# Kernel tuning notes

Measured on AMD Instinct MI355X. Metric: run time of the kernel, lower is better.

## Reference

```python
import jax, jax.numpy as jnp
import numpy as np

HEADS = 16
KEY_SIZE = 64
HEAD_SIZE = 64
D_MODEL = 1024
MASK_BIG = 1e12


def setup_inputs() -> dict:
    key = jax.random.key(0)
    ks = jax.random.split(key, 16)
    B, S, D = 4, 2048, D_MODEL
    qk_dim = HEADS * KEY_SIZE
    out_dim = HEADS * HEAD_SIZE
    s = 0.02
    return {
        'q': jax.random.normal(ks[0], (B, S, D), jnp.float32),
        'k': jax.random.normal(ks[1], (B, S, D), jnp.float32),
        'v': jax.random.normal(ks[2], (B, S, D), jnp.float32),
        'q_mask': jax.random.randint(ks[3], (B, S), 0, 2, jnp.int32),
        'v_mask': jax.random.randint(ks[4], (B, S), 0, 2, jnp.int32),
        'Wq': jax.random.normal(ks[5], (D, qk_dim), jnp.float32) * s,
        'bq': jnp.zeros((qk_dim,), jnp.float32),
        'Wk': jax.random.normal(ks[6], (D, qk_dim), jnp.float32) * s,
        'bk': jnp.zeros((qk_dim,), jnp.float32),
        'Wv': jax.random.normal(ks[7], (D, out_dim), jnp.float32) * s,
        'bv': jnp.zeros((out_dim,), jnp.float32),
        'Wo': jax.random.normal(ks[8], (out_dim, out_dim), jnp.float32) * s,
        'bo': jnp.zeros((out_dim,), jnp.float32),
    }


def reference(q, k, v, q_mask, v_mask, Wq, bq, Wk, bk, Wv, bv, Wo, bo):
    B, Sq, _ = q.shape
    Sk = k.shape[1]
    # projections -> [B, H, S, d]
    qw = (q @ Wq + bq).reshape(B, Sq, HEADS, KEY_SIZE).transpose(0, 2, 1, 3)
    kw = (k @ Wk + bk).reshape(B, Sk, HEADS, KEY_SIZE).transpose(0, 2, 1, 3)
    vw = (v @ Wv + bv).reshape(B, Sk, HEADS, HEAD_SIZE).transpose(0, 2, 1, 3)
    # scaled dot-product scores [B, H, Sq, Sk]
    a = jnp.einsum('bhqd,bhkd->bhqk', qw, kw) / np.sqrt(KEY_SIZE).astype(np.float32)
    # v_mask: additive -inf-like penalty on padded keys (mode=1, axis=-1)
    vm = v_mask.astype(a.dtype)[:, None, None, :]
    a = a - (1.0 - vm) * MASK_BIG
    # a_mask=True: causal mask (mask future positions)
    causal = jnp.tril(jnp.ones((Sq, Sk), a.dtype))
    a = a - (1.0 - causal) * MASK_BIG
    a = jax.nn.softmax(a, axis=-1)
    # attention output [B, Sq, H*head_size]
    o = jnp.einsum('bhqk,bhkd->bhqd', a, vw).transpose(0, 2, 1, 3).reshape(B, Sq, HEADS * HEAD_SIZE)
    o = o @ Wo + bo
    # q_mask: multiplicative zeroing of padded query outputs (mode=0, axis=1)
    o = o * q_mask.astype(o.dtype)[:, :, None]
    return o
```

## Files before the change

kernel.cpp:

```cpp
#include <hip/hip_runtime.h>
#include <hip/hip_bf16.h>

typedef __attribute__((ext_vector_type(8))) short v8s;
typedef __attribute__((ext_vector_type(4))) float v4f;
typedef __attribute__((ext_vector_type(16))) float v16f;
typedef __attribute__((ext_vector_type(4))) unsigned v4u;

#define S_LEN 2048
#define NB 4
#define NH 16
#define LOG2E 1.4426950408889634f
#define CMASK 1443109011456.0f
#define DEFER_THR 11.55f

__device__ __forceinline__ short f2bf(float f) {
    __hip_bfloat16 h = __float2bfloat16(f);
    union { __hip_bfloat16 h; short s; } u; u.h = h; return u.s;
}

__device__ __forceinline__ unsigned cvtpk(float lo, float hi) {
    unsigned r;
    asm("v_cvt_pk_bf16_f32 %0, %1, %2" : "=v"(r) : "v"(lo), "v"(hi));
    return r;
}

__device__ __forceinline__ int swz(int row, int col) {
    return (row * 128 + col) ^ ((row & 7) << 4);
}

__device__ __forceinline__ void async16(void* lds, const void* g) {
    __builtin_amdgcn_global_load_lds(
        (const __attribute__((address_space(1))) unsigned int*)g,
        (__attribute__((address_space(3))) unsigned int*)lds, 16, 0, 0);
}

#define MFMA16(a, b, c) __builtin_amdgcn_mfma_f32_16x16x32_bf16((a), (b), (c), 0, 0, 0)
#define MFMA32(a, b, c) __builtin_amdgcn_mfma_f32_32x32x16_bf16((a), (b), (c), 0, 0, 0)

__global__ __launch_bounds__(256) void convert_all(const float* __restrict__ q,
                                                   const float* __restrict__ k,
                                                   const float* __restrict__ v,
                                                   short* __restrict__ Xq,
                                                   short* __restrict__ Xk,
                                                   short* __restrict__ Xv,
                                                   float* __restrict__ outz) {
    if (blockIdx.y == 3) {
        size_t i = ((size_t)blockIdx.x * 256 + threadIdx.x) * 8;
        float4 z4 = {0.f, 0.f, 0.f, 0.f};
        *(float4*)(outz + i) = z4;
        *(float4*)(outz + i + 4) = z4;
        return;
    }
    const float* in = (blockIdx.y == 0) ? q : (blockIdx.y == 1) ? k : v;
    short* out = (blockIdx.y == 0) ? Xq : (blockIdx.y == 1) ? Xk : Xv;
    size_t i = ((size_t)blockIdx.x * 256 + threadIdx.x) * 8;
    float4 a = *(const float4*)(in + i);
    float4 b = *(const float4*)(in + i + 4);
    v8s o;
    o[0] = f2bf(a.x); o[1] = f2bf(a.y); o[2] = f2bf(a.z); o[3] = f2bf(a.w);
    o[4] = f2bf(b.x); o[5] = f2bf(b.y); o[6] = f2bf(b.z); o[7] = f2bf(b.w);
    *(v8s*)(out + i) = o;
}

__global__ __launch_bounds__(256) void build_pen(const int* __restrict__ vm,
                                                 short* __restrict__ penC) {
    int i = blockIdx.x * 256 + threadIdx.x;
    penC[i] = vm[i] ? (short)0 : f2bf(-CMASK);
}

__global__ __launch_bounds__(256) void compact_qmask(const int* __restrict__ qm,
                                                     int* __restrict__ idx,
                                                     int* __restrict__ nq) {
    const int b = blockIdx.x;
    const int* m = qm + b * S_LEN;
    int* ib = idx + b * S_LEN;
    __shared__ int cnt[256];
    const int t = threadIdx.x;
    int loc[8], c = 0;
#pragma unroll
    for (int i = 0; i < 8; ++i) { int s = t * 8 + i; if (m[s]) loc[c++] = s; }
    cnt[t] = c;
    __syncthreads();
    for (int d = 1; d < 256; d <<= 1) {
        int v = (t >= d) ? cnt[t - d] : 0;
        __syncthreads();
        cnt[t] += v;
        __syncthreads();
    }
    int off = cnt[t] - c;
    for (int i = 0; i < c; ++i) ib[off + i] = loc[i];
    if (t == 255) nq[b] = cnt[255];
}

__global__ __launch_bounds__(256) void transpose_all(const float* __restrict__ Wq,
                                                     const float* __restrict__ Wk,
                                                     const float* __restrict__ Wv,
                                                     const float* __restrict__ Wo,
                                                     short* __restrict__ WTq,
                                                     short* __restrict__ WTk,
                                                     short* __restrict__ WTv,
                                                     short* __restrict__ WTo) {
    const int z = blockIdx.z;
    const float* W = (z == 0) ? Wq : (z == 1) ? Wk : (z == 2) ? Wv : Wo;
    short* WT = (z == 0) ? WTq : (z == 1) ? WTk : (z == 2) ? WTv : WTo;
    __shared__ float tile[32][33];
    int k0 = blockIdx.x * 32, n0 = blockIdx.y * 32;
    int tx = threadIdx.x & 31, ty = threadIdx.x >> 5;
#pragma unroll
    for (int i = 0; i < 4; ++i)
        tile[ty + i * 8][tx] = W[(size_t)(k0 + ty + i * 8) * 1024 + n0 + tx];
    __syncthreads();
#pragma unroll
    for (int i = 0; i < 4; ++i)
        WT[(size_t)(n0 + ty + i * 8) * 1024 + k0 + tx] = f2bf(tile[tx][ty + i * 8]);
}

__global__ __launch_bounds__(512)
void proj_all(const short* __restrict__ Xk, const short* __restrict__ Xv,
              const short* __restrict__ Xq,
              const short* __restrict__ WTk, const short* __restrict__ WTv,
              const short* __restrict__ WTq,
              const float* __restrict__ bk, const float* __restrict__ bv,
              const float* __restrict__ bq,
              const int* __restrict__ idx, const int* __restrict__ nq,
              short* __restrict__ KF, short* __restrict__ VF,
              short* __restrict__ QW) {
    __shared__ short As[2][128 * 64];
    __shared__ short Bs[2][128 * 64];
    const int tid = threadIdx.x;
    const int l = tid & 63, w = tid >> 6;
    const int g = l >> 4, ql = l & 15;
    const int z = blockIdx.z;
    const int bid = blockIdx.x;
    const int y = (bid & 7) + 8 * (bid >> 6);
    const int n0 = ((bid >> 3) & 7) * 128;
    const int wr = w >> 2, wc = w & 3;

    int b = 0, m0 = y * 128, m0c = 0, nqv = 0;
    const int* idxb = nullptr;
    if (z == 2) {
        if (y >= 36) return;
        b = y / 9; m0c = (y % 9) * 128;
        nqv = nq[b];
        if (m0c >= nqv) return;
        idxb = idx + b * S_LEN;
    }
    const short* A  = (z == 0) ? Xk : (z == 1) ? Xv : Xq;
    const short* BT = (z == 0) ? WTk : (z == 1) ? WTv : WTq;
    const float* bias = (z == 0) ? bk : (z == 1) ? bv : bq;

    int arow[2];
#pragma unroll
    for (int i = 0; i < 2; ++i) {
        int row = (i * 512 + tid) >> 3;
        if (z == 2) {
            int jc = m0c + row;
            arow[i] = b * S_LEN + idxb[(jc < nqv) ? jc : (nqv - 1)];
        } else {
            arow[i] = m0 + row;
        }
    }
    const int c8 = (((l & 7) ^ (l >> 3))) * 8;

    v4f acc[4][2] = {};

    auto stage = [&](int kt, int buf) {
        const int kk = kt * 64;
#pragma unroll
        for (int i = 0; i < 2; ++i) {
            int ci = i * 512 + tid;
            async16((char*)As[buf] + (size_t)ci * 16,
                    A + (size_t)arow[i] * 1024 + kk + c8);
            async16((char*)Bs[buf] + (size_t)ci * 16,
                    BT + (size_t)(n0 + (ci >> 3)) * 1024 + kk + c8);
        }
    };

    stage(0, 0);
    for (int kt = 0; kt < 16; ++kt) {
        __builtin_amdgcn_s_barrier();
        __builtin_amdgcn_sched_barrier(0);
        if (kt + 1 < 16) {
            stage(kt + 1, (kt + 1) & 1);
            asm volatile("s_waitcnt vmcnt(4)" ::: "memory");
        } else {
            asm volatile("s_waitcnt vmcnt(0)" ::: "memory");
        }
        __builtin_amdgcn_sched_barrier(0);
        __builtin_amdgcn_s_barrier();
        __builtin_amdgcn_sched_barrier(0);
        const short* Ab = As[kt & 1];
        const short* Bb = Bs[kt & 1];
#pragma unroll
        for (int ks = 0; ks < 2; ++ks) {
            v8s af[4], bfr[2];
#pragma unroll
            for (int mt = 0; mt < 4; ++mt)
                af[mt] = *(const v8s*)((char*)Ab +
                          swz(wr * 64 + mt * 16 + ql, ks * 64 + g * 16));
#pragma unroll
            for (int nt = 0; nt < 2; ++nt)
                bfr[nt] = *(const v8s*)((char*)Bb +
                          swz(wc * 32 + nt * 16 + ql, ks * 64 + g * 16));
#pragma unroll
            for (int mt = 0; mt < 4; ++mt)
#pragma unroll
                for (int nt = 0; nt < 2; ++nt)
                    acc[mt][nt] = MFMA16(af[mt], bfr[nt], acc[mt][nt]);
        }
    }

#pragma unroll
    for (int nt = 0; nt < 2; ++nt) {
        int col = n0 + wc * 32 + nt * 16 + ql;
        float bval = bias[col];
        int hh = col >> 6, dd = col & 63;
#pragma unroll
        for (int mt = 0; mt < 4; ++mt) {
#pragma unroll
            for (int r = 0; r < 4; ++r) {
                int lrow = wr * 64 + mt * 16 + g * 4 + r;
                float vv = acc[mt][nt][r] + bval;
                if (z == 0) {
                    int gm = m0 + lrow;
                    int bb = gm >> 11, ss = gm & 2047;
                    size_t base = (size_t)(bb * NH + hh) * 131072
                                + (size_t)(ss >> 6) * 4096
                                + (dd >> 4) * 1024 + (ss & 63) * 16
                                + ((dd >> 3) & 1) * 8 + (dd & 7);
                    KF[base] = f2bf(vv);
                } else if (z == 1) {
                    int gm = m0 + lrow;
                    int bb = gm >> 11, ss = gm & 2047;
                    int wkp = ss & 63;
                    size_t base = (size_t)(bb * NH + hh) * 131072
                                + (size_t)(ss >> 6) * 4096
                                + (wkp >> 4) * 1024 + dd * 16
                                + ((wkp >> 3) & 1) * 8 + (wkp & 7);
                    VF[base] = f2bf(vv);
                } else {
                    int jc = m0c + lrow;
                    vv *= 0.125f * LOG2E;
                    QW[((size_t)(b * NH + hh) * S_LEN + jc) * 64 + dd] = f2bf(vv);
                }
            }
        }
    }
}

__global__ __launch_bounds__(64)
void attn_kernel(const short* __restrict__ QW, const short* __restrict__ KF,
                 const short* __restrict__ VF, const short* __restrict__ penC,
                 const int* __restrict__ idx, const int* __restrict__ nq,
                 short* __restrict__ O) {
    const int l = threadIdx.x;
    const int lq = l & 31, hi = l >> 5;
    const int bh = blockIdx.x;
    const int chunk = 63 - (int)blockIdx.y;
    const int b = bh >> 4, hd = bh & 15;

    const int nqv = nq[b];
    const int cy = chunk * 32;
    if (cy >= nqv) return;

    const short* Qp = QW + (size_t)bh * S_LEN * 64;
    const short* Kp = KF + (size_t)bh * 131072;
    const short* Vp = VF + (size_t)bh * 131072;
    const short* pp = penC + b * S_LEN;
    const int* idxb = idx + b * S_LEN;

    const int j = cy + lq;
    const int jj = (j < nqv) ? j : (nqv - 1);
    const int q_glob = idxb[jj];
    const int qmin = __builtin_amdgcn_readfirstlane(q_glob);

    int lastj = cy + 31; if (lastj > nqv - 1) lastj = nqv - 1;
    const int NT = (idxb[lastj] >> 6) + 1;

    v8s qf[4];
#pragma unroll
    for (int ks = 0; ks < 4; ++ks)
        qf[ks] = *(const v8s*)(Qp + (size_t)jj * 64 + ks * 16 + hi * 8);
    v8s qf4 = {};
    qf4[0] = hi ? (short)0 : (short)0x3F80;

    v16f accO[2] = {};
    float m_run = -INFINITY, l_run = 0.f;

    auto tile = [&](int kt, bool causal) {
        const int k0 = kt * 64;
        const short* Kt = Kp + (size_t)kt * 4096;
        const short* Vt = Vp + (size_t)kt * 4096;
        short p0 = pp[k0 + lq], p1 = pp[k0 + lq + 32];

        v8s kf0[4], kf1[4];
#pragma unroll
        for (int ks = 0; ks < 4; ++ks) {
            kf0[ks] = *(const v8s*)(Kt + ks * 1024 + lq * 16 + hi * 8);
            kf1[ks] = *(const v8s*)(Kt + ks * 1024 + (lq + 32) * 16 + hi * 8);
        }
        v16f acc0 = {}, acc1 = {};
        __builtin_amdgcn_s_setprio(1);
#pragma unroll
        for (int ks = 0; ks < 4; ++ks) {
            acc0 = MFMA32(kf0[ks], qf[ks], acc0);
            acc1 = MFMA32(kf1[ks], qf[ks], acc1);
        }
        v8s k4a = {}, k4b = {};
        k4a[0] = hi ? (short)0 : p0;
        k4b[0] = hi ? (short)0 : p1;
        acc0 = MFMA32(k4a, qf4, acc0);
        acc1 = MFMA32(k4b, qf4, acc1);
        __builtin_amdgcn_s_setprio(0);

        float s[32];
#pragma unroll
        for (int jn = 0; jn < 16; ++jn) { s[jn] = acc0[jn]; s[16 + jn] = acc1[jn]; }
        if (causal) {
#pragma unroll
            for (int t = 0; t < 2; ++t)
#pragma unroll
                for (int jn = 0; jn < 16; ++jn) {
                    int kp = k0 + t * 32 + (jn & 3) + 8 * (jn >> 2) + 4 * hi;
                    if (kp > q_glob) s[t * 16 + jn] -= CMASK;
                }
        }
        float t8[8];
#pragma unroll
        for (int i = 0; i < 8; ++i)
            t8[i] = fmaxf(fmaxf(s[i], s[i + 8]), fmaxf(s[i + 16], s[i + 24]));
#pragma unroll
        for (int i = 0; i < 4; ++i) t8[i] = fmaxf(t8[i], t8[i + 4]);
        float tmax = fmaxf(fmaxf(t8[0], t8[1]), fmaxf(t8[2], t8[3]));
        tmax = fmaxf(tmax, __shfl_xor(tmax, 32, 64));

        if (__any(tmax > m_run + DEFER_THR)) {
            float mnew = fmaxf(m_run, tmax);
            float scale = exp2f(m_run - mnew);
            m_run = mnew;
            l_run *= scale;
#pragma unroll
            for (int jn = 0; jn < 16; ++jn) {
                float sc = __shfl(scale, (jn & 3) + 8 * (jn >> 2) + 4 * hi, 64);
                accO[0][jn] *= sc;
                accO[1][jn] *= sc;
            }
        }
#pragma unroll
        for (int i = 0; i < 32; ++i) s[i] = exp2f(s[i] - m_run);
        float u8[8];
#pragma unroll
        for (int i = 0; i < 8; ++i)
            u8[i] = (s[i] + s[i + 8]) + (s[i + 16] + s[i + 24]);
#pragma unroll
        for (int i = 0; i < 4; ++i) u8[i] += u8[i + 4];
        float psum = (u8[0] + u8[1]) + (u8[2] + u8[3]);
        psum += __shfl_xor(psum, 32, 64);
        l_run += psum;

        v8s vf0[4], vf1[4];
#pragma unroll
        for (int ks = 0; ks < 4; ++ks) {
            vf0[ks] = *(const v8s*)(Vt + ks * 1024 + lq * 16 + hi * 8);
            vf1[ks] = *(const v8s*)(Vt + ks * 1024 + (lq + 32) * 16 + hi * 8);
        }

        v8s PA[4];
#pragma unroll
        for (int t = 0; t < 2; ++t)
#pragma unroll
            for (int sf = 0; sf < 2; ++sf) {
                int base = t * 16 + sf * 8;
                unsigned x0 = cvtpk(s[base + 0], s[base + 1]);
                unsigned x1 = cvtpk(s[base + 2], s[base + 3]);
                unsigned y0 = cvtpk(s[base + 4], s[base + 5]);
                unsigned y1 = cvtpk(s[base + 6], s[base + 7]);
                asm volatile("v_permlane32_swap_b32 %0, %1" : "+v"(x0), "+v"(y0));
                asm volatile("v_permlane32_swap_b32 %0, %1" : "+v"(x1), "+v"(y1));
                v4u wv; wv[0] = x0; wv[1] = x1; wv[2] = y0; wv[3] = y1;
                union { v4u u; v8s s8; } cvt; cvt.u = wv;
                PA[t * 2 + sf] = cvt.s8;
            }

        __builtin_amdgcn_s_setprio(1);
#pragma unroll
        for (int ks = 0; ks < 4; ++ks) {
            accO[0] = MFMA32(PA[ks], vf0[ks], accO[0]);
            accO[1] = MFMA32(PA[ks], vf1[ks], accO[1]);
        }
        __builtin_amdgcn_s_setprio(0);
    };

    for (int kt = 0; kt < NT; ++kt)
        tile(kt, kt * 64 + 63 > qmin);

    int kt = NT;
    while (kt < 32 && __any(m_run < -1e11f)) {
        tile(kt, true);
        ++kt;
    }

    float inv = 1.0f / l_run;
#pragma unroll
    for (int jn = 0; jn < 16; ++jn) {
        int rowq = (jn & 3) + 8 * (jn >> 2) + 4 * hi;
        float iv = __shfl(inv, rowq, 64);
        int jrow = cy + rowq;
        if (jrow < nqv) {
            size_t base = (size_t)(b * S_LEN + jrow) * 1024 + hd * 64 + lq;
            O[base]      = f2bf(accO[0][jn] * iv);
            O[base + 32] = f2bf(accO[1][jn] * iv);
        }
    }
}

__global__ __launch_bounds__(512)
void out_gemm_c(const short* __restrict__ A, const short* __restrict__ BT,
                const float* __restrict__ bias, const int* __restrict__ idx,
                const int* __restrict__ nq, float* __restrict__ out) {
    __shared__ short As[2][128 * 64];
    __shared__ short Bs[2][128 * 64];
    const int tid = threadIdx.x;
    const int l = tid & 63, w = tid >> 6;
    const int g = l >> 4, ql = l & 15;
    const int bid = blockIdx.x;
    const int y = (bid & 7) + 8 * (bid >> 6);
    if (y >= 36) return;
    const int n0 = ((bid >> 3) & 7) * 128;
    const int b = y / 9;
    const int m0c = (y % 9) * 128;
    const int nqv = nq[b];
    if (m0c >= nqv) return;
    const int* idxb = idx + b * S_LEN;
    const int wr = w >> 2, wc = w & 3;
    const int c8 = (((l & 7) ^ (l >> 3))) * 8;

    v4f acc[4][2] = {};

    auto stage = [&](int kt, int buf) {
        const int kk = kt * 64;
#pragma unroll
        for (int i = 0; i < 2; ++i) {
            int ci = i * 512 + tid;
            int row = ci >> 3;
            async16((char*)As[buf] + (size_t)ci * 16,
                    A + (size_t)(b * S_LEN + m0c + row) * 1024 + kk + c8);
            async16((char*)Bs[buf] + (size_t)ci * 16,
                    BT + (size_t)(n0 + row) * 1024 + kk + c8);
        }
    };

    stage(0, 0);
    for (int kt = 0; kt < 16; ++kt) {
        __builtin_amdgcn_s_barrier();
        __builtin_amdgcn_sched_barrier(0);
        if (kt + 1 < 16) {
            stage(kt + 1, (kt + 1) & 1);
            asm volatile("s_waitcnt vmcnt(4)" ::: "memory");
        } else {
            asm volatile("s_waitcnt vmcnt(0)" ::: "memory");
        }
        __builtin_amdgcn_sched_barrier(0);
        __builtin_amdgcn_s_barrier();
        __builtin_amdgcn_sched_barrier(0);
        const short* Ab = As[kt & 1];
        const short* Bb = Bs[kt & 1];
#pragma unroll
        for (int ks = 0; ks < 2; ++ks) {
            v8s af[4], bfr[2];
#pragma unroll
            for (int mt = 0; mt < 4; ++mt)
                af[mt] = *(const v8s*)((char*)Ab +
                          swz(wr * 64 + mt * 16 + ql, ks * 64 + g * 16));
#pragma unroll
            for (int nt = 0; nt < 2; ++nt)
                bfr[nt] = *(const v8s*)((char*)Bb +
                          swz(wc * 32 + nt * 16 + ql, ks * 64 + g * 16));
#pragma unroll
            for (int mt = 0; mt < 4; ++mt)
#pragma unroll
                for (int nt = 0; nt < 2; ++nt)
                    acc[mt][nt] = MFMA16(af[mt], bfr[nt], acc[mt][nt]);
        }
    }

#pragma unroll
    for (int nt = 0; nt < 2; ++nt) {
        int col = n0 + wc * 32 + nt * 16 + ql;
        float bval = bias[col];
#pragma unroll
        for (int mt = 0; mt < 4; ++mt) {
#pragma unroll
            for (int r = 0; r < 4; ++r) {
                int jc = m0c + wr * 64 + mt * 16 + g * 4 + r;
                if (jc < nqv) {
                    int orig = idxb[jc];
                    out[(size_t)(b * S_LEN + orig) * 1024 + col] =
                        acc[mt][nt][r] + bval;
                }
            }
        }
    }
}

extern "C" void kernel_launch(void* const* d_in, const int* in_sizes, int n_in,
                              void* d_out, int out_size, void* d_ws, size_t ws_size,
                              hipStream_t stream) {
    (void)in_sizes; (void)n_in; (void)out_size; (void)ws_size;
    const float* q  = (const float*)d_in[0];
    const float* k  = (const float*)d_in[1];
    const float* v  = (const float*)d_in[2];
    const int* qmask = (const int*)d_in[3];
    const int* vmask = (const int*)d_in[4];
    const float* Wq = (const float*)d_in[5];
    const float* bq = (const float*)d_in[6];
    const float* Wk = (const float*)d_in[7];
    const float* bk = (const float*)d_in[8];
    const float* Wv = (const float*)d_in[9];
    const float* bv = (const float*)d_in[10];
    const float* Wo = (const float*)d_in[11];
    const float* bo = (const float*)d_in[12];
    float* out = (float*)d_out;

    char* ws = (char*)d_ws;
    const size_t MB = 1024 * 1024;
    short* Xq  = (short*)(ws + 0 * MB);
    short* Xk  = (short*)(ws + 16 * MB);
    short* Xv  = (short*)(ws + 32 * MB);
    short* WTq = (short*)(ws + 48 * MB);
    short* WTk = (short*)(ws + 50 * MB);
    short* WTv = (short*)(ws + 52 * MB);
    short* WTo = (short*)(ws + 54 * MB);
    short* QW  = (short*)(ws + 56 * MB);
    short* KF  = (short*)(ws + 72 * MB);
    short* VFb = (short*)(ws + 88 * MB);
    short* Ob  = (short*)(ws + 104 * MB);
    short* penC = (short*)(ws + 120 * MB);
    int* idxB  = (int*)(ws + 121 * MB);
    int* nqB   = (int*)(ws + 122 * MB);

    convert_all<<<dim3(4096, 4), 256, 0, stream>>>(q, k, v, Xq, Xk, Xv, out);
    transpose_all<<<dim3(32, 32, 4), 256, 0, stream>>>(Wq, Wk, Wv, Wo,
                                                       WTq, WTk, WTv, WTo);
    build_pen<<<32, 256, 0, stream>>>(vmask, penC);
    compact_qmask<<<NB, 256, 0, stream>>>(qmask, idxB, nqB);

    proj_all<<<dim3(512, 1, 3), 512, 0, stream>>>(Xk, Xv, Xq, WTk, WTv, WTq,
                                                  bk, bv, bq, idxB, nqB,
                                                  KF, VFb, QW);
    attn_kernel<<<dim3(64, 64), 64, 0, stream>>>(QW, KF, VFb, penC, idxB, nqB, Ob);
    out_gemm_c<<<320, 512, 0, stream>>>(Ob, WTo, bo, idxB, nqB, out);
}
```

Before: 211.5 us.

## Split long causal attention chunks across two blocks with a combine kernel

Query chunks that span more than eight key tiles are split into two halves of the key range, each processed by its own block. Each half writes its partial max, sum and unnormalized output (bf16) to workspace, and a new combine kernel merges them with log-sum-exp rescaling. This is meant to balance the triangular causal workload and raise parallelism on the long chunks. The cost is an extra launch, extra global traffic, and bf16 rounding of the partial accumulators. Split pieces skip the fallback loop for fully masked rows, which may change results for those rows.

```diff
diff --git a/kernel.cpp b/kernel.cpp
--- a/kernel.cpp
+++ b/kernel.cpp
@@ -16,6 +16,10 @@
 __device__ __forceinline__ short f2bf(float f) {
     __hip_bfloat16 h = __float2bfloat16(f);
     union { __hip_bfloat16 h; short s; } u; u.h = h; return u.s;
+}
+__device__ __forceinline__ float bf2f(short s) {
+    union { unsigned u; float f; } u; u.u = ((unsigned)(unsigned short)s) << 16;
+    return u.f;
 }
 
 __device__ __forceinline__ unsigned cvtpk(float lo, float hi) {
@@ -252,11 +256,15 @@
 void attn_kernel(const short* __restrict__ QW, const short* __restrict__ KF,
                  const short* __restrict__ VF, const short* __restrict__ penC,
                  const int* __restrict__ idx, const int* __restrict__ nq,
-                 short* __restrict__ O) {
+                 short* __restrict__ O,
+                 float* __restrict__ mP, float* __restrict__ lP,
+                 short* __restrict__ accP) {
     const int l = threadIdx.x;
     const int lq = l & 31, hi = l >> 5;
     const int bh = blockIdx.x;
-    const int chunk = 63 - (int)blockIdx.y;
+    const int y = blockIdx.y;
+    const int piece = y & 1;
+    const int chunk = 63 - (y >> 1);
     const int b = bh >> 4, hd = bh & 15;
 
     const int nqv = nq[b];
@@ -276,6 +284,11 @@
 
     int lastj = cy + 31; if (lastj > nqv - 1) lastj = nqv - 1;
     const int NT = (idxb[lastj] >> 6) + 1;
+    const bool split = (NT > 8);
+    if (!split && piece) return;
+    const int H = NT >> 1;
+    const int t0 = split ? (piece ? H : 0) : 0;
+    const int t1 = split ? (piece ? NT : H) : NT;
 
     v8s qf[4];
 #pragma unroll
@@ -391,10 +404,26 @@
         __builtin_amdgcn_s_setprio(0);
     };
 
-    for (int kt = 0; kt < NT; ++kt)
+    for (int kt = t0; kt < t1; ++kt)
         tile(kt, kt * 64 + 63 > qmin);
 
-    int kt = NT;
+    if (split) {
+        const int pidx = (bh * 64 + chunk) * 2 + piece;
+        if (hi == 0) {
+            mP[(size_t)pidx * 32 + lq] = m_run;
+            lP[(size_t)pidx * 32 + lq] = l_run;
+        }
+        short* aPp = accP + (size_t)pidx * 2048;
+#pragma unroll
+        for (int jn = 0; jn < 16; ++jn) {
+            int rowq = (jn & 3) + 8 * (jn >> 2) + 4 * hi;
+            aPp[rowq * 64 + lq]      = f2bf(accO[0][jn]);
+            aPp[rowq * 64 + 32 + lq] = f2bf(accO[1][jn]);
+        }
+        return;
+    }
+
+    int kt = t1;
     while (kt < 32 && __any(m_run < -1e11f)) {
         tile(kt, true);
         ++kt;
@@ -411,6 +440,40 @@
             O[base]      = f2bf(accO[0][jn] * iv);
             O[base + 32] = f2bf(accO[1][jn] * iv);
         }
+    }
+}
+
+__global__ __launch_bounds__(64)
+void attn_combine(const float* __restrict__ mP, const float* __restrict__ lP,
+                  const short* __restrict__ accP, const int* __restrict__ idx,
+                  const int* __restrict__ nq, short* __restrict__ O) {
+    const int bh = blockIdx.x, chunk = blockIdx.y;
+    const int b = bh >> 4, hd = bh & 15;
+    const int nqv = nq[b];
+    const int cy = chunk * 32;
+    if (cy >= nqv) return;
+    const int* idxb = idx + b * S_LEN;
+    int lastj = cy + 31; if (lastj > nqv - 1) lastj = nqv - 1;
+    const int NT = (idxb[lastj] >> 6) + 1;
+    if (NT <= 8) return;
+
+    const int lane = threadIdx.x;
+    const int p0 = (bh * 64 + chunk) * 2;
+    const float* m0 = mP + (size_t)p0 * 32;  const float* m1 = m0 + 32;
+    const float* l0 = lP + (size_t)p0 * 32;  const float* l1 = l0 + 32;
+    const short* a0 = accP + (size_t)p0 * 2048;
+    const short* a1 = a0 + 2048;
+
+    for (int r = 0; r < 32; ++r) {
+        int jrow = cy + r;
+        if (jrow >= nqv) break;
+        float ma = m0[r], mb = m1[r];
+        float m = fmaxf(ma, mb);
+        float s0 = exp2f(ma - m), s1 = exp2f(mb - m);
+        float lsum = l0[r] * s0 + l1[r] * s1;
+        float o = (bf2f(a0[r * 64 + lane]) * s0 + bf2f(a1[r * 64 + lane]) * s1)
+                  / lsum;
+        O[(size_t)(b * S_LEN + jrow) * 1024 + hd * 64 + lane] = f2bf(o);
     }
 }
 
@@ -538,6 +601,9 @@
     short* penC = (short*)(ws + 120 * MB);
     int* idxB  = (int*)(ws + 121 * MB);
     int* nqB   = (int*)(ws + 122 * MB);
+    short* accP = (short*)(ws + 0 * MB);
+    float* mP   = (float*)(ws + 34 * MB);
+    float* lP   = (float*)(ws + 37 * MB);
 
     convert_all<<<dim3(4096, 4), 256, 0, stream>>>(q, k, v, Xq, Xk, Xv, out);
     transpose_all<<<dim3(32, 32, 4), 256, 0, stream>>>(Wq, Wk, Wv, Wo,
@@ -548,6 +614,8 @@
     proj_all<<<dim3(512, 1, 3), 512, 0, stream>>>(Xk, Xv, Xq, WTk, WTv, WTq,
                                                   bk, bv, bq, idxB, nqB,
                                                   KF, VFb, QW);
-    attn_kernel<<<dim3(64, 64), 64, 0, stream>>>(QW, KF, VFb, penC, idxB, nqB, Ob);
+    attn_kernel<<<dim3(64, 128), 64, 0, stream>>>(QW, KF, VFb, penC, idxB, nqB,
+                                                  Ob, mP, lP, accP);
+    attn_combine<<<dim3(64, 64), 64, 0, stream>>>(mP, lP, accP, idxB, nqB, Ob);
     out_gemm_c<<<320, 512, 0, stream>>>(Ob, WTo, bo, idxB, nqB, out);
 }
```

Measured after the change: 240.8 us. 13.9% more time.
